# Optimization experiments

Hardware: AMD Instinct MI355X
Metric: run time of the kernel (lower is better)

Reference implementation:

```python
import jax, jax.numpy as jnp
import numpy as np

T = 10
NUM_HEADS = 12

def _rel_pos_index(t):
    coords = jnp.arange(t)
    return coords[:, None] - coords[None, :] + (t - 1)  # [T, T] in [0, 2T-2]

def setup_inputs() -> dict:
    key = jax.random.key(0)
    ks = jax.random.split(key, 6)
    dim, attn_dim = 384, 384
    B_ = 16384
    return {
        "x": jax.random.normal(ks[0], (B_, T, dim), dtype=jnp.float32),
        "qkv_w": jax.random.normal(ks[1], (3 * attn_dim, dim), dtype=jnp.float32) * 0.02,
        "qkv_b": jax.random.normal(ks[2], (3 * attn_dim,), dtype=jnp.float32) * 0.02,
        "proj_w": jax.random.normal(ks[3], (dim, attn_dim), dtype=jnp.float32) * 0.02,
        "proj_b": jax.random.normal(ks[4], (dim,), dtype=jnp.float32) * 0.02,
        "bias_table": jax.random.normal(ks[5], (2 * T - 1, NUM_HEADS), dtype=jnp.float32) * 0.02,
    }

def reference(x, qkv_w, qkv_b, proj_w, proj_b, bias_table):
    B_, N, C = x.shape
    H = NUM_HEADS
    Dh = qkv_w.shape[0] // (3 * H)
    scale = Dh ** -0.5
    qkv = x @ qkv_w.T + qkv_b                       # [B_, N, 3*H*Dh]
    qkv = qkv.reshape(B_, N, 3, H, Dh).transpose(2, 0, 3, 1, 4)
    q, k, v = qkv[0], qkv[1], qkv[2]                # each [B_, H, N, Dh]
    idx = _rel_pos_index(N)                         # [N, N]
    bias = bias_table[idx].transpose(2, 0, 1)       # [H, N, N]
    attn = jnp.einsum('bhnd,bhmd->bhnm', q * scale, k) + bias[None]
    attn = jax.nn.softmax(attn, axis=-1)
    out = jnp.einsum('bhnm,bhmd->bhnd', attn, v)    # [B_, H, N, Dh]
    out = out.transpose(0, 2, 1, 3).reshape(B_, N, H * Dh)
    return out @ proj_w.T + proj_b
```

## Files before the change

### kernel.cpp

```cpp
#include <hip/hip_runtime.h>
#include <cstdint>
#include <cstddef>

#define T_TOK 10
#define NH 12
#define DH 32
#define DIM 384
#define QKVDIM 1152
#define NB 4
#define MROWS 40
#define XS_LD 392
#define QK_LD 776
#define SCALE 0.17677669529663689f

#define QK_OFF   37632
#define VT_OFF   99712
#define BIAS_OFF 148864
#define LDS_BYTES 149776

typedef short bf16x8 __attribute__((ext_vector_type(8)));
typedef float f32x4  __attribute__((ext_vector_type(4)));

__device__ __forceinline__ unsigned short f2b(float f) {
    unsigned u = __float_as_uint(f);
    u = (u + 0x7FFFu + ((u >> 16) & 1u)) >> 16;
    return (unsigned short)u;
}
__device__ __forceinline__ unsigned pack2(float a, float b) {
    return (unsigned)f2b(a) | ((unsigned)f2b(b) << 16);
}

__global__ void convert_weights(const float* __restrict__ qkv_w,
                                const float* __restrict__ proj_w,
                                unsigned short* __restrict__ wq,
                                unsigned short* __restrict__ wp) {
    int i = blockIdx.x * blockDim.x + threadIdx.x;
    const int N1 = QKVDIM * DIM / 4;
    const int N2 = DIM * DIM / 4;
    if (i < N1) {
        float4 v = ((const float4*)qkv_w)[i];
        uint2 o; o.x = pack2(v.x, v.y); o.y = pack2(v.z, v.w);
        ((uint2*)wq)[i] = o;
    } else if (i < N1 + N2) {
        int j = i - N1;
        float4 v = ((const float4*)proj_w)[j];
        uint2 o; o.x = pack2(v.x, v.y); o.y = pack2(v.z, v.w);
        ((uint2*)wp)[j] = o;
    }
}

extern __shared__ char smem[];

__global__ __launch_bounds__(512, 2) void fused_attn(
    const float* __restrict__ x,
    const float* __restrict__ qkv_b,
    const float* __restrict__ proj_b,
    const float* __restrict__ bias_table,
    const unsigned short* __restrict__ wq,
    const unsigned short* __restrict__ wp,
    float* __restrict__ out)
{
    const int t    = threadIdx.x;
    const int wg   = blockIdx.x;
    const int wave = t >> 6;
    const int lane = t & 63;
    const int quad = lane >> 4;
    const int l16  = lane & 15;

    unsigned short* xs       = (unsigned short*)smem;
    unsigned short* qk       = (unsigned short*)(smem + QK_OFF);
    unsigned short* vt       = (unsigned short*)(smem + VT_OFF);
    float*          outstage = (float*)(smem + QK_OFF);
    float*          bias_lds = (float*)(smem + BIAS_OFF);

    {
        const float4* x4 = (const float4*)(x + (size_t)wg * MROWS * DIM);
        for (int idx = t; idx < MROWS * 96; idx += 512) {
            int row = idx / 96, c4 = idx % 96;
            float4 v = x4[idx];
            uint2 o; o.x = pack2(v.x, v.y); o.y = pack2(v.z, v.w);
            *(uint2*)(xs + row * XS_LD + c4 * 4) = o;
        }
        for (int idx = t; idx < 8 * 96; idx += 512) {
            int row = MROWS + idx / 96, c4 = idx % 96;
            *(uint2*)(xs + row * XS_LD + c4 * 4) = make_uint2(0u, 0u);
        }
        for (int idx = t; idx < 3072; idx += 512)
            ((uint4*)vt)[idx] = make_uint4(0u, 0u, 0u, 0u);
        if (t < (2 * T_TOK - 1) * NH) bias_lds[t] = bias_table[t];
    }
    __syncthreads();

    {
        #pragma unroll 1
        for (int g = 0; g < 3; ++g) {
            f32x4 acc[3][3] = {};
            #pragma unroll
            for (int kc = 0; kc < 12; ++kc) {
                int koff = kc * 32 + quad * 8;
                bf16x8 a0 = *(const bf16x8*)(xs + ( 0 + l16) * XS_LD + koff);
                bf16x8 a1 = *(const bf16x8*)(xs + (16 + l16) * XS_LD + koff);
                bf16x8 a2 = *(const bf16x8*)(xs + (32 + l16) * XS_LD + koff);
                bf16x8 b0 = *(const bf16x8*)(wq + (size_t)((wave + 8*(3*g+0))*16 + l16) * DIM + koff);
                bf16x8 b1 = *(const bf16x8*)(wq + (size_t)((wave + 8*(3*g+1))*16 + l16) * DIM + koff);
                bf16x8 b2 = *(const bf16x8*)(wq + (size_t)((wave + 8*(3*g+2))*16 + l16) * DIM + koff);
                acc[0][0] = __builtin_amdgcn_mfma_f32_16x16x32_bf16(a0, b0, acc[0][0], 0, 0, 0);
                acc[0][1] = __builtin_amdgcn_mfma_f32_16x16x32_bf16(a0, b1, acc[0][1], 0, 0, 0);
                acc[0][2] = __builtin_amdgcn_mfma_f32_16x16x32_bf16(a0, b2, acc[0][2], 0, 0, 0);
                acc[1][0] = __builtin_amdgcn_mfma_f32_16x16x32_bf16(a1, b0, acc[1][0], 0, 0, 0);
                acc[1][1] = __builtin_amdgcn_mfma_f32_16x16x32_bf16(a1, b1, acc[1][1], 0, 0, 0);
                acc[1][2] = __builtin_amdgcn_mfma_f32_16x16x32_bf16(a1, b2, acc[1][2], 0, 0, 0);
                acc[2][0] = __builtin_amdgcn_mfma_f32_16x16x32_bf16(a2, b0, acc[2][0], 0, 0, 0);
                acc[2][1] = __builtin_amdgcn_mfma_f32_16x16x32_bf16(a2, b1, acc[2][1], 0, 0, 0);
                acc[2][2] = __builtin_amdgcn_mfma_f32_16x16x32_bf16(a2, b2, acc[2][2], 0, 0, 0);
            }
            #pragma unroll
            for (int j = 0; j < 3; ++j) {
                int n = (wave + 8*(3*g+j)) * 16 + l16;
                float qb = qkv_b[n];
                if (g < 2) {
                    float sc = (g == 0) ? SCALE : 1.0f;
                    #pragma unroll
                    for (int mt = 0; mt < 3; ++mt) {
                        #pragma unroll
                        for (int r = 0; r < 4; ++r) {
                            int m = mt * 16 + quad * 4 + r;
                            if (m < MROWS)
                                qk[m * QK_LD + n] = f2b((acc[mt][j][r] + qb) * sc);
                        }
                    }
                } else {
                    int h = (n - 2*DIM) >> 5;
                    int d = (n - 2*DIM) & 31;
                    #pragma unroll
                    for (int mt = 0; mt < 3; ++mt) {
                        #pragma unroll
                        for (int r = 0; r < 4; ++r) {
                            int m = mt * 16 + quad * 4 + r;
                            if (m < MROWS) {
                                int bl = (m * 205) >> 11;
                                int jt = m - bl * 10;
                                vt[((bl*NH + h)*DH + d)*16 + jt] = f2b(acc[mt][j][r] + qb);
                            }
                        }
                    }
                }
            }
        }
    }
    __syncthreads();

    {
        const int l16c = (l16 < T_TOK) ? l16 : (T_TOK - 1);
        const int joff = (quad < 2) ? quad * 8 : 8;
        #pragma unroll 2
        for (int pp = 0; pp < 6; ++pp) {
            int p  = wave * 6 + pp;
            int bl = p / NH, h = p % NH;
            int rowq = bl * T_TOK + l16c;
            bf16x8 kf = *(const bf16x8*)(qk + rowq * QK_LD + DIM + h * DH + quad * 8);
            bf16x8 qf = *(const bf16x8*)(qk + rowq * QK_LD +       h * DH + quad * 8);
            f32x4 sv = {};
            sv = __builtin_amdgcn_mfma_f32_16x16x32_bf16(kf, qf, sv, 0, 0, 0);
            float s[4];
            #pragma unroll
            for (int r = 0; r < 4; ++r) {
                int jj  = quad * 4 + r;
                int jjc = (jj < T_TOK) ? jj : (T_TOK - 1);
                float b = bias_lds[(l16c - jjc + T_TOK - 1) * NH + h];
                s[r] = (jj < T_TOK) ? (sv[r] + b) : -1.0e30f;
            }
            float mx = fmaxf(fmaxf(s[0], s[1]), fmaxf(s[2], s[3]));
            mx = fmaxf(mx, __shfl_xor(mx, 16));
            mx = fmaxf(mx, __shfl_xor(mx, 32));
            float p0 = __expf(s[0] - mx), p1 = __expf(s[1] - mx);
            float p2 = __expf(s[2] - mx), p3 = __expf(s[3] - mx);
            float sl = p0 + p1 + p2 + p3;
            sl += __shfl_xor(sl, 16);
            sl += __shfl_xor(sl, 32);
            float rinv = 1.0f / sl;
            unsigned w0 = pack2(p0, p1), w1 = pack2(p2, p3);
            int s0l = ((quad & 1) << 5) + l16;
            unsigned d0 = (unsigned)__shfl((int)w0, s0l);
            unsigned d1 = (unsigned)__shfl((int)w1, s0l);
            unsigned d2 = (unsigned)__shfl((int)w0, s0l + 16);
            unsigned d3 = (unsigned)__shfl((int)w1, s0l + 16);
            if (quad >= 2) { d0 = 0; d1 = 0; d2 = 0; d3 = 0; }
            union { bf16x8 v; unsigned u[4]; } pa;
            pa.u[0] = d0; pa.u[1] = d1; pa.u[2] = d2; pa.u[3] = d3;
            const unsigned short* vb = vt + (size_t)((bl*NH + h)*DH) * 16;
            bf16x8 v0 = *(const bf16x8*)(vb + ( 0 + l16) * 16 + joff);
            bf16x8 v1 = *(const bf16x8*)(vb + (16 + l16) * 16 + joff);
            f32x4 o0 = {}, o1 = {};
            o0 = __builtin_amdgcn_mfma_f32_16x16x32_bf16(pa.v, v0, o0, 0, 0, 0);
            o1 = __builtin_amdgcn_mfma_f32_16x16x32_bf16(pa.v, v1, o1, 0, 0, 0);
            #pragma unroll
            for (int r = 0; r < 4; ++r) {
                float rv = __shfl(rinv, quad * 4 + r);
                int i = quad * 4 + r;
                if (i < T_TOK) {
                    int m = bl * T_TOK + i;
                    xs[m * XS_LD + h * DH +      l16] = f2b(o0[r] * rv);
                    xs[m * XS_LD + h * DH + 16 + l16] = f2b(o1[r] * rv);
                }
            }
        }
    }
    __syncthreads();

    {
        f32x4 acc[3][3] = {};
        #pragma unroll
        for (int kc = 0; kc < 12; ++kc) {
            int koff = kc * 32 + quad * 8;
            bf16x8 a0 = *(const bf16x8*)(xs + ( 0 + l16) * XS_LD + koff);
            bf16x8 a1 = *(const bf16x8*)(xs + (16 + l16) * XS_LD + koff);
            bf16x8 a2 = *(const bf16x8*)(xs + (32 + l16) * XS_LD + koff);
            bf16x8 b0 = *(const bf16x8*)(wp + (size_t)((wave +  0)*16 + l16) * DIM + koff);
            bf16x8 b1 = *(const bf16x8*)(wp + (size_t)((wave +  8)*16 + l16) * DIM + koff);
            bf16x8 b2 = *(const bf16x8*)(wp + (size_t)((wave + 16)*16 + l16) * DIM + koff);
            acc[0][0] = __builtin_amdgcn_mfma_f32_16x16x32_bf16(a0, b0, acc[0][0], 0, 0, 0);
            acc[0][1] = __builtin_amdgcn_mfma_f32_16x16x32_bf16(a0, b1, acc[0][1], 0, 0, 0);
            acc[0][2] = __builtin_amdgcn_mfma_f32_16x16x32_bf16(a0, b2, acc[0][2], 0, 0, 0);
            acc[1][0] = __builtin_amdgcn_mfma_f32_16x16x32_bf16(a1, b0, acc[1][0], 0, 0, 0);
            acc[1][1] = __builtin_amdgcn_mfma_f32_16x16x32_bf16(a1, b1, acc[1][1], 0, 0, 0);
            acc[1][2] = __builtin_amdgcn_mfma_f32_16x16x32_bf16(a1, b2, acc[1][2], 0, 0, 0);
            acc[2][0] = __builtin_amdgcn_mfma_f32_16x16x32_bf16(a2, b0, acc[2][0], 0, 0, 0);
            acc[2][1] = __builtin_amdgcn_mfma_f32_16x16x32_bf16(a2, b1, acc[2][1], 0, 0, 0);
            acc[2][2] = __builtin_amdgcn_mfma_f32_16x16x32_bf16(a2, b2, acc[2][2], 0, 0, 0);
        }
        #pragma unroll
        for (int j = 0; j < 3; ++j) {
            int c = (wave + 8*j) * 16 + l16;
            #pragma unroll
            for (int mt = 0; mt < 3; ++mt) {
                #pragma unroll
                for (int r = 0; r < 4; ++r) {
                    int m = mt * 16 + quad * 4 + r;
                    if (m < MROWS)
                        outstage[m * DIM + c] = acc[mt][j][r];
                }
            }
        }
    }
    __syncthreads();

    {
        const float4* st4 = (const float4*)outstage;
        const float4* pb4 = (const float4*)proj_b;
        float4* out4 = (float4*)(out + (size_t)wg * MROWS * DIM);
        for (int idx = t; idx < MROWS * 96; idx += 512) {
            int c4 = idx % 96;
            float4 v = st4[idx];
            float4 b = pb4[c4];
            float4 r; r.x = v.x + b.x; r.y = v.y + b.y; r.z = v.z + b.z; r.w = v.w + b.w;
            out4[idx] = r;
        }
    }
}

extern "C" void kernel_launch(void* const* d_in, const int* in_sizes, int n_in,
                              void* d_out, int out_size, void* d_ws, size_t ws_size,
                              hipStream_t stream) {
    const float* x          = (const float*)d_in[0];
    const float* qkv_b      = (const float*)d_in[1];
    const float* qkv_b_     = (const float*)d_in[2];
    const float* proj_w     = (const float*)d_in[3];
    const float* proj_b     = (const float*)d_in[4];
    const float* bias_table = (const float*)d_in[5];
    const float* qkv_w = qkv_b;
    const float* qkv_bias = qkv_b_;

    unsigned short* wq = (unsigned short*)d_ws;
    unsigned short* wp = wq + (size_t)QKVDIM * DIM;
    float* out = (float*)d_out;

    convert_weights<<<576, 256, 0, stream>>>(qkv_w, proj_w, wq, wp);

    hipFuncSetAttribute((const void*)fused_attn,
                        hipFuncAttributeMaxDynamicSharedMemorySize, LDS_BYTES);
    fused_attn<<<16384 / NB, 512, LDS_BYTES, stream>>>(x, qkv_bias, proj_b, bias_table, wq, wp, out);
}
```

Baseline: 1.075 ms.

## Make fused attention kernel persistent with register-prefetched x tiles

Replaces the one-block-per-tile grid with 256 persistent blocks that each loop over 16 tiles. The next tile's x is prefetched into registers during the attention and projection phases, and biases are held in registers. Output is written directly from the accumulators with the bias added, dropping the LDS staging pass, and the V-transposed layout gets an XOR swizzle to reduce bank conflicts. The risk is that 256 blocks may underfill the GPU, and the 32 extra float4 prefetch registers raise register pressure.

```diff
diff --git a/kernel.cpp b/kernel.cpp
--- a/kernel.cpp
+++ b/kernel.cpp
@@ -12,6 +12,8 @@
 #define XS_LD 392
 #define QK_LD 776
 #define SCALE 0.17677669529663689f
+#define NBLK 256
+#define NIT  16
 
 #define QK_OFF   37632
 #define VT_OFF   99712
@@ -61,7 +63,7 @@
     float* __restrict__ out)
 {
     const int t    = threadIdx.x;
-    const int wg   = blockIdx.x;
+    const int b    = blockIdx.x;
     const int wave = t >> 6;
     const int lane = t & 63;
     const int quad = lane >> 4;
@@ -70,30 +72,180 @@
     unsigned short* xs       = (unsigned short*)smem;
     unsigned short* qk       = (unsigned short*)(smem + QK_OFF);
     unsigned short* vt       = (unsigned short*)(smem + VT_OFF);
-    float*          outstage = (float*)(smem + QK_OFF);
     float*          bias_lds = (float*)(smem + BIAS_OFF);
 
+    float pb[3];
+    float qbr[3][3];
+    #pragma unroll
+    for (int j = 0; j < 3; ++j) pb[j] = proj_b[(wave + 8*j) * 16 + l16];
+    #pragma unroll
+    for (int g = 0; g < 3; ++g)
+        #pragma unroll
+        for (int j = 0; j < 3; ++j)
+            qbr[g][j] = qkv_b[(wave + 8*(3*g+j)) * 16 + l16];
+
+    for (int idx = t; idx < 8 * 96; idx += 512) {
+        int row = MROWS + idx / 96, c4 = idx % 96;
+        *(uint2*)(xs + row * XS_LD + c4 * 4) = make_uint2(0u, 0u);
+    }
+    for (int idx = t; idx < 3072; idx += 512)
+        ((uint4*)vt)[idx] = make_uint4(0u, 0u, 0u, 0u);
+    if (t < (2 * T_TOK - 1) * NH) bias_lds[t] = bias_table[t];
+
+    float4 px[8];
     {
-        const float4* x4 = (const float4*)(x + (size_t)wg * MROWS * DIM);
-        for (int idx = t; idx < MROWS * 96; idx += 512) {
-            int row = idx / 96, c4 = idx % 96;
-            float4 v = x4[idx];
-            uint2 o; o.x = pack2(v.x, v.y); o.y = pack2(v.z, v.w);
-            *(uint2*)(xs + row * XS_LD + c4 * 4) = o;
-        }
-        for (int idx = t; idx < 8 * 96; idx += 512) {
-            int row = MROWS + idx / 96, c4 = idx % 96;
-            *(uint2*)(xs + row * XS_LD + c4 * 4) = make_uint2(0u, 0u);
-        }
-        for (int idx = t; idx < 3072; idx += 512)
-            ((uint4*)vt)[idx] = make_uint4(0u, 0u, 0u, 0u);
-        if (t < (2 * T_TOK - 1) * NH) bias_lds[t] = bias_table[t];
+        const float4* xg = (const float4*)(x + (size_t)b * MROWS * DIM);
+        #pragma unroll
+        for (int i = 0; i < 8; ++i) {
+            int idx = i * 512 + t;
+            if (idx < MROWS * 96) px[i] = xg[idx];
+        }
     }
-    __syncthreads();
-
-    {
-        #pragma unroll 1
-        for (int g = 0; g < 3; ++g) {
+
+    for (int it = 0; it < NIT; ++it) {
+        const size_t g = (size_t)it * NBLK + b;
+
+        #pragma unroll
+        for (int i = 0; i < 8; ++i) {
+            int idx = i * 512 + t;
+            if (idx < MROWS * 96) {
+                int row = idx / 96, c4 = idx % 96;
+                uint2 o; o.x = pack2(px[i].x, px[i].y); o.y = pack2(px[i].z, px[i].w);
+                *(uint2*)(xs + row * XS_LD + c4 * 4) = o;
+            }
+        }
+        __syncthreads();
+
+        {
+            #pragma unroll 1
+            for (int gg = 0; gg < 3; ++gg) {
+                f32x4 acc[3][3] = {};
+                #pragma unroll
+                for (int kc = 0; kc < 12; ++kc) {
+                    int koff = kc * 32 + quad * 8;
+                    bf16x8 a0 = *(const bf16x8*)(xs + ( 0 + l16) * XS_LD + koff);
+                    bf16x8 a1 = *(const bf16x8*)(xs + (16 + l16) * XS_LD + koff);
+                    bf16x8 a2 = *(const bf16x8*)(xs + (32 + l16) * XS_LD + koff);
+                    bf16x8 b0 = *(const bf16x8*)(wq + (size_t)((wave + 8*(3*gg+0))*16 + l16) * DIM + koff);
+                    bf16x8 b1 = *(const bf16x8*)(wq + (size_t)((wave + 8*(3*gg+1))*16 + l16) * DIM + koff);
+                    bf16x8 b2 = *(const bf16x8*)(wq + (size_t)((wave + 8*(3*gg+2))*16 + l16) * DIM + koff);
+                    acc[0][0] = __builtin_amdgcn_mfma_f32_16x16x32_bf16(a0, b0, acc[0][0], 0, 0, 0);
+                    acc[0][1] = __builtin_amdgcn_mfma_f32_16x16x32_bf16(a0, b1, acc[0][1], 0, 0, 0);
+                    acc[0][2] = __builtin_amdgcn_mfma_f32_16x16x32_bf16(a0, b2, acc[0][2], 0, 0, 0);
+                    acc[1][0] = __builtin_amdgcn_mfma_f32_16x16x32_bf16(a1, b0, acc[1][0], 0, 0, 0);
+                    acc[1][1] = __builtin_amdgcn_mfma_f32_16x16x32_bf16(a1, b1, acc[1][1], 0, 0, 0);
+                    acc[1][2] = __builtin_amdgcn_mfma_f32_16x16x32_bf16(a1, b2, acc[1][2], 0, 0, 0);
+                    acc[2][0] = __builtin_amdgcn_mfma_f32_16x16x32_bf16(a2, b0, acc[2][0], 0, 0, 0);
+                    acc[2][1] = __builtin_amdgcn_mfma_f32_16x16x32_bf16(a2, b1, acc[2][1], 0, 0, 0);
+                    acc[2][2] = __builtin_amdgcn_mfma_f32_16x16x32_bf16(a2, b2, acc[2][2], 0, 0, 0);
+                }
+                #pragma unroll
+                for (int j = 0; j < 3; ++j) {
+                    int n = (wave + 8*(3*gg+j)) * 16 + l16;
+                    float qb = qbr[gg][j];
+                    if (gg < 2) {
+                        float sc = (gg == 0) ? SCALE : 1.0f;
+                        #pragma unroll
+                        for (int mt = 0; mt < 3; ++mt) {
+                            #pragma unroll
+                            for (int r = 0; r < 4; ++r) {
+                                int m = mt * 16 + quad * 4 + r;
+                                if (m < MROWS)
+                                    qk[m * QK_LD + n] = f2b((acc[mt][j][r] + qb) * sc);
+                            }
+                        }
+                    } else {
+                        int h = (n - 2*DIM) >> 5;
+                        int d = (n - 2*DIM) & 31;
+                        int sd = ((d >> 2) & 1) << 3;
+                        #pragma unroll
+                        for (int mt = 0; mt < 3; ++mt) {
+                            #pragma unroll
+                            for (int r = 0; r < 4; ++r) {
+                                int m = mt * 16 + quad * 4 + r;
+                                if (m < MROWS) {
+                                    int bl = (m * 205) >> 11;
+                                    int jt = m - bl * 10;
+                                    vt[((bl*NH + h)*DH + d)*16 + (jt ^ sd)] = f2b(acc[mt][j][r] + qb);
+                                }
+                            }
+                        }
+                    }
+                }
+            }
+        }
+        __syncthreads();
+
+        {
+            const int l16c = (l16 < T_TOK) ? l16 : (T_TOK - 1);
+            const int joff = (quad < 2) ? quad * 8 : 8;
+            const int sw   = ((l16 >> 2) & 1) << 3;
+            const int joff2 = joff ^ sw;
+            #pragma unroll 2
+            for (int pp = 0; pp < 6; ++pp) {
+                int p  = wave * 6 + pp;
+                int bl = p / NH, h = p % NH;
+                int rowq = bl * T_TOK + l16c;
+                bf16x8 kf = *(const bf16x8*)(qk + rowq * QK_LD + DIM + h * DH + quad * 8);
+                bf16x8 qf = *(const bf16x8*)(qk + rowq * QK_LD +       h * DH + quad * 8);
+                f32x4 sv = {};
+                sv = __builtin_amdgcn_mfma_f32_16x16x32_bf16(kf, qf, sv, 0, 0, 0);
+                float s[4];
+                #pragma unroll
+                for (int r = 0; r < 4; ++r) {
+                    int jj  = quad * 4 + r;
+                    int jjc = (jj < T_TOK) ? jj : (T_TOK - 1);
+                    float bb = bias_lds[(l16c - jjc + T_TOK - 1) * NH + h];
+                    s[r] = (jj < T_TOK) ? (sv[r] + bb) : -1.0e30f;
+                }
+                float mx = fmaxf(fmaxf(s[0], s[1]), fmaxf(s[2], s[3]));
+                mx = fmaxf(mx, __shfl_xor(mx, 16));
+                mx = fmaxf(mx, __shfl_xor(mx, 32));
+                float p0 = __expf(s[0] - mx), p1 = __expf(s[1] - mx);
+                float p2 = __expf(s[2] - mx), p3 = __expf(s[3] - mx);
+                float sl = p0 + p1 + p2 + p3;
+                sl += __shfl_xor(sl, 16);
+                sl += __shfl_xor(sl, 32);
+                float rinv = 1.0f / sl;
+                unsigned w0 = pack2(p0, p1), w1 = pack2(p2, p3);
+                int s0l = ((quad & 1) << 5) + l16;
+                unsigned d0 = (unsigned)__shfl((int)w0, s0l);
+                unsigned d1 = (unsigned)__shfl((int)w1, s0l);
+                unsigned d2 = (unsigned)__shfl((int)w0, s0l + 16);
+                unsigned d3 = (unsigned)__shfl((int)w1, s0l + 16);
+                if (quad >= 2) { d0 = 0; d1 = 0; d2 = 0; d3 = 0; }
+                union { bf16x8 v; unsigned u[4]; } pa;
+                pa.u[0] = d0; pa.u[1] = d1; pa.u[2] = d2; pa.u[3] = d3;
+                const unsigned short* vb = vt + (size_t)((bl*NH + h)*DH) * 16;
+                bf16x8 v0 = *(const bf16x8*)(vb + ( 0 + l16) * 16 + joff2);
+                bf16x8 v1 = *(const bf16x8*)(vb + (16 + l16) * 16 + joff2);
+                f32x4 o0 = {}, o1 = {};
+                o0 = __builtin_amdgcn_mfma_f32_16x16x32_bf16(pa.v, v0, o0, 0, 0, 0);
+                o1 = __builtin_amdgcn_mfma_f32_16x16x32_bf16(pa.v, v1, o1, 0, 0, 0);
+                #pragma unroll
+                for (int r = 0; r < 4; ++r) {
+                    float rv = __shfl(rinv, quad * 4 + r);
+                    int i = quad * 4 + r;
+                    if (i < T_TOK) {
+                        int m = bl * T_TOK + i;
+                        xs[m * XS_LD + h * DH +      l16] = f2b(o0[r] * rv);
+                        xs[m * XS_LD + h * DH + 16 + l16] = f2b(o1[r] * rv);
+                    }
+                }
+            }
+        }
+
+        if (it + 1 < NIT) {
+            const float4* xg = (const float4*)(x + ((size_t)(it+1) * NBLK + b) * MROWS * DIM);
+            #pragma unroll
+            for (int i = 0; i < 8; ++i) {
+                int idx = i * 512 + t;
+                if (idx < MROWS * 96) px[i] = xg[idx];
+            }
+        }
+        __syncthreads();
+
+        {
             f32x4 acc[3][3] = {};
             #pragma unroll
             for (int kc = 0; kc < 12; ++kc) {
@@ -101,9 +253,9 @@
                 bf16x8 a0 = *(const bf16x8*)(xs + ( 0 + l16) * XS_LD + koff);
                 bf16x8 a1 = *(const bf16x8*)(xs + (16 + l16) * XS_LD + koff);
                 bf16x8 a2 = *(const bf16x8*)(xs + (32 + l16) * XS_LD + koff);
-                bf16x8 b0 = *(const bf16x8*)(wq + (size_t)((wave + 8*(3*g+0))*16 + l16) * DIM + koff);
-                bf16x8 b1 = *(const bf16x8*)(wq + (size_t)((wave + 8*(3*g+1))*16 + l16) * DIM + koff);
-                bf16x8 b2 = *(const bf16x8*)(wq + (size_t)((wave + 8*(3*g+2))*16 + l16) * DIM + koff);
+                bf16x8 b0 = *(const bf16x8*)(wp + (size_t)((wave +  0)*16 + l16) * DIM + koff);
+                bf16x8 b1 = *(const bf16x8*)(wp + (size_t)((wave +  8)*16 + l16) * DIM + koff);
+                bf16x8 b2 = *(const bf16x8*)(wp + (size_t)((wave + 16)*16 + l16) * DIM + koff);
                 acc[0][0] = __builtin_amdgcn_mfma_f32_16x16x32_bf16(a0, b0, acc[0][0], 0, 0, 0);
                 acc[0][1] = __builtin_amdgcn_mfma_f32_16x16x32_bf16(a0, b1, acc[0][1], 0, 0, 0);
                 acc[0][2] = __builtin_amdgcn_mfma_f32_16x16x32_bf16(a0, b2, acc[0][2], 0, 0, 0);
@@ -114,148 +266,23 @@
                 acc[2][1] = __builtin_amdgcn_mfma_f32_16x16x32_bf16(a2, b1, acc[2][1], 0, 0, 0);
                 acc[2][2] = __builtin_amdgcn_mfma_f32_16x16x32_bf16(a2, b2, acc[2][2], 0, 0, 0);
             }
+            float* og = out + g * (MROWS * DIM);
             #pragma unroll
             for (int j = 0; j < 3; ++j) {
-                int n = (wave + 8*(3*g+j)) * 16 + l16;
-                float qb = qkv_b[n];
-                if (g < 2) {
-                    float sc = (g == 0) ? SCALE : 1.0f;
+                int c = (wave + 8*j) * 16 + l16;
+                float pbv = pb[j];
+                #pragma unroll
+                for (int mt = 0; mt < 3; ++mt) {
                     #pragma unroll
-                    for (int mt = 0; mt < 3; ++mt) {
-                        #pragma unroll
-                        for (int r = 0; r < 4; ++r) {
-                            int m = mt * 16 + quad * 4 + r;
-                            if (m < MROWS)
-                                qk[m * QK_LD + n] = f2b((acc[mt][j][r] + qb) * sc);
-                        }
+                    for (int r = 0; r < 4; ++r) {
+                        int m = mt * 16 + quad * 4 + r;
+                        if (m < MROWS)
+                            og[m * DIM + c] = acc[mt][j][r] + pbv;
                     }
-                } else {
-                    int h = (n - 2*DIM) >> 5;
-                    int d = (n - 2*DIM) & 31;
-                    #pragma unroll
-                    for (int mt = 0; mt < 3; ++mt) {
-                        #pragma unroll
-                        for (int r = 0; r < 4; ++r) {
-                            int m = mt * 16 + quad * 4 + r;
-                            if (m < MROWS) {
-                                int bl = (m * 205) >> 11;
-                                int jt = m - bl * 10;
-                                vt[((bl*NH + h)*DH + d)*16 + jt] = f2b(acc[mt][j][r] + qb);
-                            }
-                        }
-                    }
-                }
-            }
-        }
-    }
-    __syncthreads();
-
-    {
-        const int l16c = (l16 < T_TOK) ? l16 : (T_TOK - 1);
-        const int joff = (quad < 2) ? quad * 8 : 8;
-        #pragma unroll 2
-        for (int pp = 0; pp < 6; ++pp) {
-            int p  = wave * 6 + pp;
-            int bl = p / NH, h = p % NH;
-            int rowq = bl * T_TOK + l16c;
-            bf16x8 kf = *(const bf16x8*)(qk + rowq * QK_LD + DIM + h * DH + quad * 8);
-            bf16x8 qf = *(const bf16x8*)(qk + rowq * QK_LD +       h * DH + quad * 8);
-            f32x4 sv = {};
-            sv = __builtin_amdgcn_mfma_f32_16x16x32_bf16(kf, qf, sv, 0, 0, 0);
-            float s[4];
-            #pragma unroll
-            for (int r = 0; r < 4; ++r) {
-                int jj  = quad * 4 + r;
-                int jjc = (jj < T_TOK) ? jj : (T_TOK - 1);
-                float b = bias_lds[(l16c - jjc + T_TOK - 1) * NH + h];
-                s[r] = (jj < T_TOK) ? (sv[r] + b) : -1.0e30f;
-            }
-            float mx = fmaxf(fmaxf(s[0], s[1]), fmaxf(s[2], s[3]));
-            mx = fmaxf(mx, __shfl_xor(mx, 16));
-            mx = fmaxf(mx, __shfl_xor(mx, 32));
-            float p0 = __expf(s[0] - mx), p1 = __expf(s[1] - mx);
-            float p2 = __expf(s[2] - mx), p3 = __expf(s[3] - mx);
-            float sl = p0 + p1 + p2 + p3;
-            sl += __shfl_xor(sl, 16);
-            sl += __shfl_xor(sl, 32);
-            float rinv = 1.0f / sl;
-            unsigned w0 = pack2(p0, p1), w1 = pack2(p2, p3);
-            int s0l = ((quad & 1) << 5) + l16;
-            unsigned d0 = (unsigned)__shfl((int)w0, s0l);
-            unsigned d1 = (unsigned)__shfl((int)w1, s0l);
-            unsigned d2 = (unsigned)__shfl((int)w0, s0l + 16);
-            unsigned d3 = (unsigned)__shfl((int)w1, s0l + 16);
-            if (quad >= 2) { d0 = 0; d1 = 0; d2 = 0; d3 = 0; }
-            union { bf16x8 v; unsigned u[4]; } pa;
-            pa.u[0] = d0; pa.u[1] = d1; pa.u[2] = d2; pa.u[3] = d3;
-            const unsigned short* vb = vt + (size_t)((bl*NH + h)*DH) * 16;
-            bf16x8 v0 = *(const bf16x8*)(vb + ( 0 + l16) * 16 + joff);
-            bf16x8 v1 = *(const bf16x8*)(vb + (16 + l16) * 16 + joff);
-            f32x4 o0 = {}, o1 = {};
-            o0 = __builtin_amdgcn_mfma_f32_16x16x32_bf16(pa.v, v0, o0, 0, 0, 0);
-            o1 = __builtin_amdgcn_mfma_f32_16x16x32_bf16(pa.v, v1, o1, 0, 0, 0);
-            #pragma unroll
-            for (int r = 0; r < 4; ++r) {
-                float rv = __shfl(rinv, quad * 4 + r);
-                int i = quad * 4 + r;
-                if (i < T_TOK) {
-                    int m = bl * T_TOK + i;
-                    xs[m * XS_LD + h * DH +      l16] = f2b(o0[r] * rv);
-                    xs[m * XS_LD + h * DH + 16 + l16] = f2b(o1[r] * rv);
-                }
-            }
-        }
-    }
-    __syncthreads();
-
-    {
-        f32x4 acc[3][3] = {};
-        #pragma unroll
-        for (int kc = 0; kc < 12; ++kc) {
-            int koff = kc * 32 + quad * 8;
-            bf16x8 a0 = *(const bf16x8*)(xs + ( 0 + l16) * XS_LD + koff);
-            bf16x8 a1 = *(const bf16x8*)(xs + (16 + l16) * XS_LD + koff);
-            bf16x8 a2 = *(const bf16x8*)(xs + (32 + l16) * XS_LD + koff);
-            bf16x8 b0 = *(const bf16x8*)(wp + (size_t)((wave +  0)*16 + l16) * DIM + koff);
-            bf16x8 b1 = *(const bf16x8*)(wp + (size_t)((wave +  8)*16 + l16) * DIM + koff);
-            bf16x8 b2 = *(const bf16x8*)(wp + (size_t)((wave + 16)*16 + l16) * DIM + koff);
-            acc[0][0] = __builtin_amdgcn_mfma_f32_16x16x32_bf16(a0, b0, acc[0][0], 0, 0, 0);
-            acc[0][1] = __builtin_amdgcn_mfma_f32_16x16x32_bf16(a0, b1, acc[0][1], 0, 0, 0);
-            acc[0][2] = __builtin_amdgcn_mfma_f32_16x16x32_bf16(a0, b2, acc[0][2], 0, 0, 0);
-            acc[1][0] = __builtin_amdgcn_mfma_f32_16x16x32_bf16(a1, b0, acc[1][0], 0, 0, 0);
-            acc[1][1] = __builtin_amdgcn_mfma_f32_16x16x32_bf16(a1, b1, acc[1][1], 0, 0, 0);
-            acc[1][2] = __builtin_amdgcn_mfma_f32_16x16x32_bf16(a1, b2, acc[1][2], 0, 0, 0);
-            acc[2][0] = __builtin_amdgcn_mfma_f32_16x16x32_bf16(a2, b0, acc[2][0], 0, 0, 0);
-            acc[2][1] = __builtin_amdgcn_mfma_f32_16x16x32_bf16(a2, b1, acc[2][1], 0, 0, 0);
-            acc[2][2] = __builtin_amdgcn_mfma_f32_16x16x32_bf16(a2, b2, acc[2][2], 0, 0, 0);
-        }
-        #pragma unroll
-        for (int j = 0; j < 3; ++j) {
-            int c = (wave + 8*j) * 16 + l16;
-            #pragma unroll
-            for (int mt = 0; mt < 3; ++mt) {
-                #pragma unroll
-                for (int r = 0; r < 4; ++r) {
-                    int m = mt * 16 + quad * 4 + r;
-                    if (m < MROWS)
-                        outstage[m * DIM + c] = acc[mt][j][r];
-                }
-            }
-        }
-    }
-    __syncthreads();
-
-    {
-        const float4* st4 = (const float4*)outstage;
-        const float4* pb4 = (const float4*)proj_b;
-        float4* out4 = (float4*)(out + (size_t)wg * MROWS * DIM);
-        for (int idx = t; idx < MROWS * 96; idx += 512) {
-            int c4 = idx % 96;
-            float4 v = st4[idx];
-            float4 b = pb4[c4];
-            float4 r; r.x = v.x + b.x; r.y = v.y + b.y; r.z = v.z + b.z; r.w = v.w + b.w;
-            out4[idx] = r;
-        }
+                }
+            }
+        }
+        __syncthreads();
     }
 }
 
@@ -263,13 +290,11 @@
                               void* d_out, int out_size, void* d_ws, size_t ws_size,
                               hipStream_t stream) {
     const float* x          = (const float*)d_in[0];
-    const float* qkv_b      = (const float*)d_in[1];
-    const float* qkv_b_     = (const float*)d_in[2];
+    const float* qkv_w      = (const float*)d_in[1];
+    const float* qkv_b      = (const float*)d_in[2];
     const float* proj_w     = (const float*)d_in[3];
     const float* proj_b     = (const float*)d_in[4];
     const float* bias_table = (const float*)d_in[5];
-    const float* qkv_w = qkv_b;
-    const float* qkv_bias = qkv_b_;
 
     unsigned short* wq = (unsigned short*)d_ws;
     unsigned short* wp = wq + (size_t)QKVDIM * DIM;
@@ -279,5 +304,5 @@
 
     hipFuncSetAttribute((const void*)fused_attn,
                         hipFuncAttributeMaxDynamicSharedMemorySize, LDS_BYTES);
-    fused_attn<<<16384 / NB, 512, LDS_BYTES, stream>>>(x, qkv_bias, proj_b, bias_table, wq, wp, out);
-}
+    fused_attn<<<NBLK, 512, LDS_BYTES, stream>>>(x, qkv_b, proj_b, bias_table, wq, wp, out);
+}
```

Result: no change. 1.074 ms (-0.1%).
